# Kernel tuning notes

Measured on AMD Instinct MI355X. Metric: run time of the kernel, lower is better.

Reference implementation:

```python
import jax, jax.numpy as jnp
import numpy as np

TOPK = 64
NUM_CLASSES = 80
ALPHA = 0.5
BETA = 2.0
EPS = 1e-7


def setup_inputs() -> dict:
    key = jax.random.key(0)
    ks = jax.random.split(key, 5)
    bs, n_points, nc, n_gt = 32, 8400, NUM_CLASSES, 128

    def make_boxes(k, lead_shape):
        k1, k2 = jax.random.split(k)
        xy = jax.random.uniform(k1, lead_shape + (2,), dtype=jnp.float32) * 600.0
        wh = jax.random.uniform(k2, lead_shape + (2,), dtype=jnp.float32) * 100.0 + 2.0
        return jnp.concatenate([xy, xy + wh], axis=-1)  # xyxy, valid boxes

    pd_scores = jax.random.normal(ks[0], (bs, n_points, nc), dtype=jnp.float32)
    pd_bboxes = make_boxes(ks[1], (bs, n_points))
    anchor_points = jax.random.uniform(ks[2], (n_points, 2), dtype=jnp.float32) * 640.0
    gt_labels = jax.random.randint(ks[3], (bs, n_gt, 1), 0, nc, dtype=jnp.int32)
    gt_bboxes = make_boxes(ks[4], (bs, n_gt))
    mask_gt = jnp.ones((bs, n_gt, 1), dtype=bool)
    return {
        "pd_scores": pd_scores,
        "pd_bboxes": pd_bboxes,
        "anchor_points": anchor_points,
        "gt_labels": gt_labels,
        "gt_bboxes": gt_bboxes,
        "mask_gt": mask_gt,
    }


def _pairwise_iou(pd_bboxes, gt_bboxes):
    """Elementwise IoU of every prediction vs every GT (xyxy), per bbox_iou(xywh=False).
    Returns (bs, n_gt, n_points)."""
    p = pd_bboxes[:, None, :, :]   # (bs, 1, n_points, 4) -> box1
    g = gt_bboxes[:, :, None, :]   # (bs, n_gt, 1, 4)     -> box2
    w1 = p[..., 2] - p[..., 0]
    h1 = p[..., 3] - p[..., 1] + EPS
    w2 = g[..., 2] - g[..., 0]
    h2 = g[..., 3] - g[..., 1] + EPS
    iw = jnp.clip(jnp.minimum(p[..., 2], g[..., 2]) - jnp.maximum(p[..., 0], g[..., 0]), 0.0)
    ih = jnp.clip(jnp.minimum(p[..., 3], g[..., 3]) - jnp.maximum(p[..., 1], g[..., 1]), 0.0)
    inter = iw * ih
    union = w1 * h1 + w2 * h2 - inter + EPS
    return inter / union


def _assign(pd_scores, pd_bboxes, gt_labels, gt_bboxes, mask_gt):
    bs, n_points, nc = pd_scores.shape
    n_gt = gt_labels.shape[1]
    labels = gt_labels[..., 0]          # (bs, n_gt) int
    valid = mask_gt[..., 0]             # (bs, n_gt) bool

    # alignment metric = (sigmoid cls score + 1e-5)^alpha * (|iou| + 1e-5)^beta
    sig = jax.nn.sigmoid(pd_scores)     # (bs, n_points, nc)
    idx = jnp.broadcast_to(labels[:, None, :], (bs, n_points, n_gt))
    cls = jnp.take_along_axis(sig, idx, axis=2)              # (bs, n_points, n_gt)
    cls = jnp.transpose(cls, (0, 2, 1))                      # (bs, n_gt, n_points)
    iou = _pairwise_iou(pd_bboxes, gt_bboxes)                # (bs, n_gt, n_points)
    align = (cls + 1e-5) ** ALPHA * (jnp.abs(iou) + 1e-5) ** BETA
    align = jnp.where(valid[:, :, None], align, 0.0)

    # top-k candidate points per GT -> positive mask (scatter set)
    _, topk_idx = jax.lax.top_k(align, TOPK)                 # (bs, n_gt, TOPK)
    bi = jnp.arange(bs)[:, None, None]
    gi = jnp.arange(n_gt)[None, :, None]
    mask_pos = jnp.zeros((bs, n_gt, n_points), dtype=bool).at[bi, gi, topk_idx].set(True)
    mask_pos = mask_pos & valid[:, :, None]

    gt_ids = jnp.where(mask_pos, jnp.arange(n_gt)[None, :, None], -1)
    target_gt_idx = jnp.maximum(jnp.max(gt_ids, axis=1), 0)  # (bs, n_points)
    assigned = jnp.any(mask_pos, axis=1)                     # (bs, n_points)

    tl = jnp.take_along_axis(labels, target_gt_idx, axis=1)
    target_labels = jnp.where(assigned, tl, 0)
    tb = jnp.take_along_axis(gt_bboxes, target_gt_idx[..., None], axis=1)  # (bs, n_points, 4)
    target_bboxes = jnp.where(assigned[..., None], tb, 0.0)
    target_scores = jax.nn.one_hot(target_labels, nc, dtype=pd_scores.dtype) * assigned[..., None]
    fg_mask = jnp.sum(mask_pos, axis=1) > 0
    return target_labels, target_bboxes, target_scores, fg_mask, target_gt_idx


def reference(pd_scores, pd_bboxes, anchor_points, gt_labels, gt_bboxes, mask_gt):
    # anchor_points is accepted per the original signature but unused by its forward
    return _assign(pd_scores, pd_bboxes, gt_labels, gt_bboxes, mask_gt)
```

## Files before the change

kernel.cpp:

```cpp
#include <hip/hip_runtime.h>
#include <math.h>

#define NPTS 8400
#define NGT  128
#define NC   80
#define BS   32
#define KSEL 64
#define FEPS 1e-7f
#define TILE  128
#define NTILE 66
#define CAPI  1024
#define CAPS  512
#define CAP   2048
#define CAPC  256
#define QCAP  2048
#define SQCAP 1024
#define OPTS  16
#define NCNT  (BS * NGT + BS * NC + BS)
#define XEX   1.9800f
#define XIN   1.9825f


__device__ __forceinline__ float sig_sqrt(float x) {
  return sqrtf(1.0f / (1.0f + expf(-x)) + 1e-5f);
}

__device__ __forceinline__ unsigned int align_key(float sc, float4 pv,
                                                  float4 gb, float a2) {
  float iw = fmaxf(fminf(pv.z, gb.z) - fmaxf(pv.x, gb.x), 0.0f);
  float ih = fmaxf(fminf(pv.w, gb.w) - fmaxf(pv.y, gb.y), 0.0f);
  float inter = iw * ih;
  float w1  = pv.z - pv.x;
  float h1  = (pv.w - pv.y) + FEPS;
  float uni = w1 * h1 + a2 - inter + FEPS;
  float iou = inter / uni;
  float t   = fabsf(iou) + 1e-5f;
  return __float_as_uint(sc * (t * t));
}

__device__ __forceinline__ void sscan512(const int* hist, int tgt, int tid, int* out3) {
  if (tid < 64) {
    int loc[8]; int ssum = 0;
    #pragma unroll
    for (int i = 0; i < 8; ++i) { loc[i] = hist[tid * 8 + i]; ssum += loc[i]; }
    int v = ssum;
    #pragma unroll
    for (int d = 1; d < 64; d <<= 1) { int t = __shfl_down(v, d); if (tid + d < 64) v += t; }
    int cum = v - ssum;
    int P = -1, need = 0, cnt = 0;
    #pragma unroll
    for (int i = 7; i >= 0; --i) {
      if (P < 0 && cum < tgt && cum + loc[i] >= tgt) { P = tid * 8 + i; need = tgt - cum; cnt = loc[i]; }
      cum += loc[i];
    }
    if (P >= 0) { out3[0] = P; out3[1] = need; out3[2] = cnt; }
  }
}

__device__ __forceinline__ void sscan128(const int* hist, int tgt, int tid, int* out3) {
  if (tid < 64) {
    int l0 = hist[2 * tid], l1 = hist[2 * tid + 1];
    int ssum = l0 + l1; int v = ssum;
    #pragma unroll
    for (int d = 1; d < 64; d <<= 1) { int t = __shfl_down(v, d); if (tid + d < 64) v += t; }
    int cum = v - ssum;
    int P = -1, nd = 0, ct = 0;
    if (cum < tgt && cum + l1 >= tgt) { P = 2 * tid + 1; nd = tgt - cum; ct = l1; }
    cum += l1;
    if (P < 0 && cum < tgt && cum + l0 >= tgt) { P = 2 * tid; nd = tgt - cum; ct = l0; }
    if (P >= 0) { out3[0] = P; out3[1] = nd; out3[2] = ct; }
  }
}

__global__ __launch_bounds__(256) void tala_cinit(int* __restrict__ cnt) {
  int i = blockIdx.x * 256 + threadIdx.x;
  if (i < NCNT) cnt[i] = 0;
}

__global__ __launch_bounds__(256) void tala_prep(
    const float* __restrict__ pd_scores,
    const float* __restrict__ pd_bboxes,
    const float* __restrict__ gt_bboxes,
    int* __restrict__ cntI, uint2* __restrict__ candI,
    int* __restrict__ cntS, int* __restrict__ scL,
    int* __restrict__ bflag, int* __restrict__ tgi)
{
  __shared__ float4 sPt[TILE];
  __shared__ float4 sGt[NGT];
  __shared__ float  sA2[NGT];
  __shared__ unsigned int qgp[QCAP];
  __shared__ float        qio[QCAP];
  __shared__ unsigned int qs[SQCAP];
  __shared__ int gcnt[NGT], gbase[NGT];
  __shared__ int ccnt[NC], cbase[NC];
  __shared__ int qn, qsn;

  const int swz = (blockIdx.x & 7) * 264 + (blockIdx.x >> 3);
  const int b   = swz / NTILE;
  const int t0  = (swz % NTILE) * TILE;
  const int tid = threadIdx.x;
  const int nv  = min(TILE, NPTS - t0);

  if (tid < 128) {
    int i = blockIdx.x * 128 + tid;
    if (i < BS * NPTS) tgi[i] = -1;
    float4 gbv = ((const float4*)gt_bboxes)[b * NGT + tid];
    sGt[tid] = gbv;
    sA2[tid] = (gbv.z - gbv.x) * ((gbv.w - gbv.y) + FEPS);
    gcnt[tid] = 0;
  } else {
    int p = tid - 128;
    if (p < nv) sPt[p] = ((const float4*)pd_bboxes)[(size_t)b * NPTS + t0 + p];
  }
  if (tid < NC) ccnt[tid] = 0;
  if (tid == 0) { qn = 0; qsn = 0; }
  __syncthreads();

  const float4* in4 = (const float4*)(pd_scores + ((size_t)b * NPTS + t0) * NC);
  for (int i = tid; i < nv * (NC / 4); i += 256) {
    float4 v = in4[i];
    if (v.x >= XEX || v.y >= XEX || v.z >= XEX || v.w >= XEX) {
      int p  = t0 + i / 20;
      int c4 = (i % 20) * 4;
      float va[4] = { v.x, v.y, v.z, v.w };
      #pragma unroll
      for (int j = 0; j < 4; ++j) {
        if (va[j] >= XEX) {
          int s = atomicAdd(&qsn, 1);
          if (s < SQCAP) qs[s] = ((unsigned int)(c4 + j) << 14) | (unsigned int)p;
        }
      }
    }
  }

  {
    const int p = tid & (TILE - 1);
    const int ghalf = tid >> 7;
    if (p < nv) {
      float4 pv = sPt[p];
      float w1h1 = (pv.z - pv.x) * ((pv.w - pv.y) + FEPS);
      for (int it = 0; it < NGT / 2; ++it) {
        int g = it * 2 + ghalf;
        float4 gbv = sGt[g];
        float iw = fminf(pv.z, gbv.z) - fmaxf(pv.x, gbv.x);
        float ih = fminf(pv.w, gbv.w) - fmaxf(pv.y, gbv.y);
        if (iw > 0.0f && ih > 0.0f) {
          float inter = iw * ih;
          float uni   = w1h1 + sA2[g] - inter + FEPS;
          float iou   = inter / uni;
          int s = atomicAdd(&qn, 1);
          if (s < QCAP) {
            qgp[s] = ((unsigned int)g << 14) | (unsigned int)(t0 + p);
            qio[s] = iou;
          }
        }
      }
    }
  }
  __syncthreads();

  int qv = min(qn, QCAP), qsv = min(qsn, SQCAP);
  if (tid == 0 && (qn > QCAP || qsn > SQCAP)) atomicOr(&bflag[b], 1);
  for (int i = tid; i < qv; i += 256) atomicAdd(&gcnt[qgp[i] >> 14], 1);
  for (int i = tid; i < qsv; i += 256) atomicAdd(&ccnt[qs[i] >> 14], 1);
  __syncthreads();
  if (tid < NGT && gcnt[tid] > 0)
    gbase[tid] = atomicAdd(&cntI[b * NGT + tid], gcnt[tid]);
  if (tid < NC && ccnt[tid] > 0)
    cbase[tid] = atomicAdd(&cntS[b * NC + tid], ccnt[tid]);
  __syncthreads();
  if (tid < NGT) gcnt[tid] = 0;
  if (tid < NC)  ccnt[tid] = 0;
  __syncthreads();
  for (int i = tid; i < qv; i += 256) {
    int g = qgp[i] >> 14, pp = qgp[i] & 16383;
    int slot = gbase[g] + atomicAdd(&gcnt[g], 1);
    if (slot < CAPI)
      candI[(size_t)(b * NGT + g) * CAPI + slot] =
          make_uint2((unsigned int)pp, __float_as_uint(qio[i]));
  }
  for (int i = tid; i < qsv; i += 256) {
    int c = qs[i] >> 14, p = qs[i] & 16383;
    int slot = cbase[c] + atomicAdd(&ccnt[c], 1);
    if (slot < CAPS) scL[(b * NC + c) * CAPS + slot] = p;
  }
}

__global__ __launch_bounds__(256, 8) void tala_sel(
    const float* __restrict__ pd_scores,
    const float* __restrict__ pd_bboxes,
    const int*   __restrict__ gt_labels,
    const float* __restrict__ gt_bboxes,
    const int*   __restrict__ cntI, const uint2* __restrict__ candI,
    const int*   __restrict__ cntS, const int*   __restrict__ scL,
    const int*   __restrict__ bflag,
    int* __restrict__ tgi)
{
  __shared__ unsigned short mp[CAP];
  __shared__ unsigned int   mk[CAP];
  __shared__ int hist[512];
  __shared__ unsigned short eqp[CAPC];
  __shared__ unsigned int   eqk[CAPC];
  __shared__ int s_bc[3];
  __shared__ int s_m, s_eqm, s_cin;

  const int swz = (blockIdx.x & 7) * 512 + (blockIdx.x >> 3);
  const int b   = swz >> 7;
  const int g   = swz & 127;
  const int tid = threadIdx.x;

  const int    label = gt_labels[b * NGT + g];
  const float4 gb    = ((const float4*)gt_bboxes)[b * NGT + g];
  const float  a2    = (gb.z - gb.x) * ((gb.w - gb.y) + FEPS);
  const float4* pb   = (const float4*)pd_bboxes + (size_t)b * NPTS;
  const float*  rawc = pd_scores + (size_t)b * NPTS * NC + label;

  const int mi = cntI[b * NGT + g];
  const int ms = cntS[b * NC + label];
  const bool listok = (mi <= CAPI) && (ms <= CAPS) && (bflag[b] == 0);

  for (int i = tid; i < 512; i += 256) hist[i] = 0;
  if (tid == 0) { s_m = listok ? mi : 0; s_eqm = 0; s_cin = 0; }
  __syncthreads();

  if (listok) {
    const uint2* lst = candI + (size_t)(b * NGT + g) * CAPI;
    for (int i = tid; i < mi; i += 256) {
      uint2 cv = lst[i];
      int p = (int)cv.x;
      float sc = sig_sqrt(rawc[(size_t)p * NC]);
      float t  = fabsf(__uint_as_float(cv.y)) + 1e-5f;
      mp[i] = (unsigned short)p;
      mk[i] = __float_as_uint(sc * (t * t));
    }
    const int* slst = scL + (b * NC + label) * CAPS;
    int cin = 0;
    for (int i = tid; i < ms; i += 256) {
      int p = slst[i];
      float x = rawc[(size_t)p * NC];
      cin += (int)(x >= XIN);
      float4 pv = pb[p];
      float iw = fminf(pv.z, gb.z) - fmaxf(pv.x, gb.x);
      float ih = fminf(pv.w, gb.w) - fmaxf(pv.y, gb.y);
      if (!(iw > 0.0f && ih > 0.0f)) {
        float sc = sig_sqrt(x);
        unsigned int k = align_key(sc, pv, gb, a2);
        int s = atomicAdd(&s_m, 1);
        mp[s] = (unsigned short)p; mk[s] = k;
      }
    }
    if (cin) atomicAdd(&s_cin, cin);
  }
  __syncthreads();

  const bool valid = listok && (s_cin >= KSEL);
  const int  m     = s_m;
  int* row = tgi + b * NPTS;
  unsigned int defGE = 0; int eqpre = -1, eqsh = 21, nd = 0;

  if (valid) {
    for (int i = tid; i < m; i += 256) atomicAdd(&hist[mk[i] >> 21], 1);
    __syncthreads();
    sscan512(hist, KSEL, tid, s_bc);
    __syncthreads();
    int P = s_bc[0], need = s_bc[1], cnt = s_bc[2];

    if (cnt == need)      { defGE = (unsigned int)P << 21;       eqpre = -1; nd = 0; }
    else if (cnt <= CAPC) { defGE = (unsigned int)(P + 1) << 21; eqpre = P; eqsh = 21; nd = need; }
    else {
      if (tid < 128) hist[tid] = 0;
      __syncthreads();
      for (int i = tid; i < m; i += 256) {
        unsigned int k = mk[i];
        if ((int)(k >> 21) == P) atomicAdd(&hist[(k >> 14) & 127], 1);
      }
      __syncthreads();
      sscan128(hist, need, tid, s_bc);
      __syncthreads();
      int Pb = s_bc[0]; nd = s_bc[1];
      eqpre = (P << 7) | Pb;
      defGE = (unsigned int)(eqpre + 1) << 14;
      eqsh  = 14;
    }
    __syncthreads();

    for (int i = tid; i < m; i += 256) {
      unsigned int k = mk[i];
      if (k >= defGE) {
        atomicMax(&row[mp[i]], g);
      } else if ((int)(k >> eqsh) == eqpre) {
        int e = atomicAdd(&s_eqm, 1);
        if (e < CAPC) { eqp[e] = mp[i]; eqk[e] = k; }
      }
    }
    __syncthreads();
  } else {
    for (int i = tid; i < 512; i += 256) hist[i] = 0;
    __syncthreads();
    for (int p = tid; p < NPTS; p += 256) {
      unsigned int k = align_key(sig_sqrt(rawc[(size_t)p * NC]), pb[p], gb, a2);
      atomicAdd(&hist[k >> 21], 1);
    }
    __syncthreads();
    sscan512(hist, KSEL, tid, s_bc);
    __syncthreads();
    int P = s_bc[0], need = s_bc[1], cnt = s_bc[2];
    if (cnt == need)      { defGE = (unsigned int)P << 21;       eqpre = -1; nd = 0; }
    else if (cnt <= CAPC) { defGE = (unsigned int)(P + 1) << 21; eqpre = P; eqsh = 21; nd = need; }
    else {
      if (tid < 128) hist[tid] = 0;
      __syncthreads();
      for (int p = tid; p < NPTS; p += 256) {
        unsigned int k = align_key(sig_sqrt(rawc[(size_t)p * NC]), pb[p], gb, a2);
        if ((int)(k >> 21) == P) atomicAdd(&hist[(k >> 14) & 127], 1);
      }
      __syncthreads();
      sscan128(hist, need, tid, s_bc);
      __syncthreads();
      int Pb = s_bc[0]; nd = s_bc[1];
      eqpre = (P << 7) | Pb;
      defGE = (unsigned int)(eqpre + 1) << 14;
      eqsh  = 14;
    }
    __syncthreads();
    for (int p = tid; p < NPTS; p += 256) {
      unsigned int k = align_key(sig_sqrt(rawc[(size_t)p * NC]), pb[p], gb, a2);
      if (k >= defGE) {
        atomicMax(&row[p], g);
      } else if ((int)(k >> eqsh) == eqpre) {
        int e = atomicAdd(&s_eqm, 1);
        if (e < CAPC) { eqp[e] = (unsigned short)p; eqk[e] = k; }
      }
    }
    __syncthreads();
  }

  int ct = min(s_eqm, CAPC);
  for (int i = tid; i < ct; i += 256) {
    unsigned int ki = eqk[i]; int pi = eqp[i];
    int r = 0;
    for (int j = 0; j < ct; ++j) {
      unsigned int kj = eqk[j];
      r += (int)((kj > ki) || (kj == ki && (int)eqp[j] < pi));
    }
    if (r < nd) atomicMax(&row[pi], g);
  }
}

__global__ __launch_bounds__(256) void tala_out(
    const int*   __restrict__ gt_labels,
    const float* __restrict__ gt_bboxes,
    float* __restrict__ out)
{
  __shared__ int s_lbl[OPTS];
  const int pt0 = blockIdx.x * OPTS;
  const int b   = pt0 / NPTS;
  const int tid = threadIdx.x;
  int* tgi = (int*)(out + (size_t)BS * NPTS * 86);

  if (tid < OPTS) {
    int idx = pt0 + tid;
    int t        = tgi[idx];
    int assigned = (t >= 0);
    int tg       = assigned ? t : 0;
    int lbl      = assigned ? gt_labels[b * NGT + tg] : 0;
    s_lbl[tid] = assigned ? lbl : -1;
    out[idx] = (float)lbl;
    float4 bb = make_float4(0.f, 0.f, 0.f, 0.f);
    if (assigned) bb = ((const float4*)gt_bboxes)[b * NGT + tg];
    ((float4*)(out + (size_t)BS * NPTS))[idx] = bb;
    out[(size_t)BS * NPTS * 85 + idx] = assigned ? 1.0f : 0.0f;
    ((float*)tgi)[idx] = (float)tg;
  }
  __syncthreads();

  float4* sc4 = (float4*)(out + (size_t)BS * NPTS * 5) + (size_t)pt0 * (NC / 4);
  #pragma unroll
  for (int j = tid; j < OPTS * (NC / 4); j += 256) {
    int lbl = s_lbl[j / (NC / 4)];
    int d   = lbl - (j % (NC / 4)) * 4;
    float4 v;
    v.x = (d == 0) ? 1.0f : 0.0f;
    v.y = (d == 1) ? 1.0f : 0.0f;
    v.z = (d == 2) ? 1.0f : 0.0f;
    v.w = (d == 3) ? 1.0f : 0.0f;
    sc4[j] = v;
  }
}

extern "C" void kernel_launch(void* const* d_in, const int* in_sizes, int n_in,
                              void* d_out, int out_size, void* d_ws, size_t ws_size,
                              hipStream_t stream) {
  const float* pd_scores = (const float*)d_in[0];
  const float* pd_bboxes = (const float*)d_in[1];
  const int*   gt_labels = (const int*)d_in[3];
  const float* gt_bboxes = (const float*)d_in[4];

  float* out = (float*)d_out;
  const size_t N = (size_t)BS * NPTS;
  int*   cntI  = (int*)(out + N);
  int*   cntS  = cntI + BS * NGT;
  int*   bflag = cntS + BS * NC;
  uint2* candI = (uint2*)(out + 5 * N);
  int*   scL   = (int*)(candI + (size_t)BS * NGT * CAPI);
  int*   tgi   = (int*)(out + 86 * N);

  tala_cinit<<<(NCNT + 255) / 256, 256, 0, stream>>>(cntI);
  tala_prep <<<BS * NTILE,      256, 0, stream>>>(pd_scores, pd_bboxes,
                                                  gt_bboxes, cntI, candI, cntS, scL,
                                                  bflag, tgi);
  tala_sel  <<<BS * NGT,        256, 0, stream>>>(pd_scores, pd_bboxes, gt_labels,
                                                  gt_bboxes, cntI, candI, cntS, scL,
                                                  bflag, tgi);
  tala_out  <<<BS * NPTS / OPTS, 256, 0, stream>>>(gt_labels, gt_bboxes, out);
}
```

Baseline: 120.2 us.

## Use wave-aggregated atomics and write IoU candidates directly to global lists

Replaces the per-thread shared-memory atomic queues with wavefront ballot aggregation, so one lane per wave performs the atomicAdd and the other lanes take slots from a prefix popcount. The IoU candidate path drops its shared staging queue and the two-pass per-GT count/scatter, and instead appends directly to the global per-GT candidate lists with one global atomic per wave per GT. This cuts shared-memory contention, LDS usage and several barriers. In exchange it adds up to 64 global atomics per wave, loses the overflow-flag signalling for the IoU queue, and makes candidate order within each list depend on wave scheduling.

Result: slower. 285.3 us (+137.3%).

```diff
diff --git a/kernel.cpp b/kernel.cpp
--- a/kernel.cpp
+++ b/kernel.cpp
@@ -13,7 +13,6 @@
 #define CAPS  512
 #define CAP   2048
 #define CAPC  256
-#define QCAP  2048
 #define SQCAP 1024
 #define OPTS  16
 #define NCNT  (BS * NGT + BS * NC + BS)
@@ -88,18 +87,16 @@
   __shared__ float4 sPt[TILE];
   __shared__ float4 sGt[NGT];
   __shared__ float  sA2[NGT];
-  __shared__ unsigned int qgp[QCAP];
-  __shared__ float        qio[QCAP];
   __shared__ unsigned int qs[SQCAP];
-  __shared__ int gcnt[NGT], gbase[NGT];
   __shared__ int ccnt[NC], cbase[NC];
-  __shared__ int qn, qsn;
-
-  const int swz = (blockIdx.x & 7) * 264 + (blockIdx.x >> 3);
-  const int b   = swz / NTILE;
-  const int t0  = (swz % NTILE) * TILE;
-  const int tid = threadIdx.x;
-  const int nv  = min(TILE, NPTS - t0);
+  __shared__ int qsn;
+
+  const int swz  = (blockIdx.x & 7) * 264 + (blockIdx.x >> 3);
+  const int b    = swz / NTILE;
+  const int t0   = (swz % NTILE) * TILE;
+  const int tid  = threadIdx.x;
+  const int lane = tid & 63;
+  const int nv   = min(TILE, NPTS - t0);
 
   if (tid < 128) {
     int i = blockIdx.x * 128 + tid;
@@ -107,78 +104,88 @@
     float4 gbv = ((const float4*)gt_bboxes)[b * NGT + tid];
     sGt[tid] = gbv;
     sA2[tid] = (gbv.z - gbv.x) * ((gbv.w - gbv.y) + FEPS);
-    gcnt[tid] = 0;
   } else {
     int p = tid - 128;
     if (p < nv) sPt[p] = ((const float4*)pd_bboxes)[(size_t)b * NPTS + t0 + p];
   }
   if (tid < NC) ccnt[tid] = 0;
-  if (tid == 0) { qn = 0; qsn = 0; }
+  if (tid == 0) qsn = 0;
   __syncthreads();
 
   const float4* in4 = (const float4*)(pd_scores + ((size_t)b * NPTS + t0) * NC);
   for (int i = tid; i < nv * (NC / 4); i += 256) {
     float4 v = in4[i];
-    if (v.x >= XEX || v.y >= XEX || v.z >= XEX || v.w >= XEX) {
-      int p  = t0 + i / 20;
-      int c4 = (i % 20) * 4;
-      float va[4] = { v.x, v.y, v.z, v.w };
-      #pragma unroll
-      for (int j = 0; j < 4; ++j) {
-        if (va[j] >= XEX) {
-          int s = atomicAdd(&qsn, 1);
-          if (s < SQCAP) qs[s] = ((unsigned int)(c4 + j) << 14) | (unsigned int)p;
+    int p  = t0 + i / 20;
+    int c4 = (i % 20) * 4;
+    float va[4] = { v.x, v.y, v.z, v.w };
+    #pragma unroll
+    for (int j = 0; j < 4; ++j) {
+      bool hit = (va[j] >= XEX);
+      unsigned long long mask = __ballot(hit);
+      if (mask) {
+        int leader = __ffsll((unsigned long long)mask) - 1;
+        int base = 0;
+        if (lane == leader) base = atomicAdd(&qsn, __popcll(mask));
+        base = __shfl(base, leader);
+        if (hit) {
+          int slot = base + __popcll(mask & ((1ull << lane) - 1ull));
+          if (slot < SQCAP) qs[slot] = ((unsigned int)(c4 + j) << 14) | (unsigned int)p;
         }
       }
     }
   }
 
   {
-    const int p = tid & (TILE - 1);
+    const int p     = tid & (TILE - 1);
     const int ghalf = tid >> 7;
-    if (p < nv) {
-      float4 pv = sPt[p];
-      float w1h1 = (pv.z - pv.x) * ((pv.w - pv.y) + FEPS);
-      for (int it = 0; it < NGT / 2; ++it) {
-        int g = it * 2 + ghalf;
-        float4 gbv = sGt[g];
+    const bool pvalid = (p < nv);
+    float4 pv = make_float4(0.f, 0.f, 0.f, 0.f);
+    float w1h1 = 0.0f;
+    if (pvalid) {
+      pv = sPt[p];
+      w1h1 = (pv.z - pv.x) * ((pv.w - pv.y) + FEPS);
+    }
+    for (int it = 0; it < NGT / 2; ++it) {
+      int g = it * 2 + ghalf;
+      float4 gbv = sGt[g];
+      bool hit = false;
+      float iou = 0.0f;
+      if (pvalid) {
         float iw = fminf(pv.z, gbv.z) - fmaxf(pv.x, gbv.x);
         float ih = fminf(pv.w, gbv.w) - fmaxf(pv.y, gbv.y);
         if (iw > 0.0f && ih > 0.0f) {
           float inter = iw * ih;
           float uni   = w1h1 + sA2[g] - inter + FEPS;
-          float iou   = inter / uni;
-          int s = atomicAdd(&qn, 1);
-          if (s < QCAP) {
-            qgp[s] = ((unsigned int)g << 14) | (unsigned int)(t0 + p);
-            qio[s] = iou;
-          }
+          iou = inter / uni;
+          hit = true;
         }
       }
-    }
-  }
-  __syncthreads();
-
-  int qv = min(qn, QCAP), qsv = min(qsn, SQCAP);
-  if (tid == 0 && (qn > QCAP || qsn > SQCAP)) atomicOr(&bflag[b], 1);
-  for (int i = tid; i < qv; i += 256) atomicAdd(&gcnt[qgp[i] >> 14], 1);
+      unsigned long long mask = __ballot(hit);
+      if (mask) {
+        int leader = __ffsll((unsigned long long)mask) - 1;
+        int base = 0;
+        if (lane == leader) base = atomicAdd(&cntI[b * NGT + g], __popcll(mask));
+        base = __shfl(base, leader);
+        if (hit) {
+          int slot = base + __popcll(mask & ((1ull << lane) - 1ull));
+          if (slot < CAPI)
+            candI[(size_t)(b * NGT + g) * CAPI + slot] =
+                make_uint2((unsigned int)(t0 + p), __float_as_uint(iou));
+        }
+      }
+    }
+  }
+  __syncthreads();
+
+  int qsv = min(qsn, SQCAP);
+  if (tid == 0 && qsn > SQCAP) atomicOr(&bflag[b], 1);
   for (int i = tid; i < qsv; i += 256) atomicAdd(&ccnt[qs[i] >> 14], 1);
   __syncthreads();
-  if (tid < NGT && gcnt[tid] > 0)
-    gbase[tid] = atomicAdd(&cntI[b * NGT + tid], gcnt[tid]);
   if (tid < NC && ccnt[tid] > 0)
     cbase[tid] = atomicAdd(&cntS[b * NC + tid], ccnt[tid]);
   __syncthreads();
-  if (tid < NGT) gcnt[tid] = 0;
-  if (tid < NC)  ccnt[tid] = 0;
-  __syncthreads();
-  for (int i = tid; i < qv; i += 256) {
-    int g = qgp[i] >> 14, pp = qgp[i] & 16383;
-    int slot = gbase[g] + atomicAdd(&gcnt[g], 1);
-    if (slot < CAPI)
-      candI[(size_t)(b * NGT + g) * CAPI + slot] =
-          make_uint2((unsigned int)pp, __float_as_uint(qio[i]));
-  }
+  if (tid < NC) ccnt[tid] = 0;
+  __syncthreads();
   for (int i = tid; i < qsv; i += 256) {
     int c = qs[i] >> 14, p = qs[i] & 16383;
     int slot = cbase[c] + atomicAdd(&ccnt[c], 1);
```
